# Kernel optimization log

Hardware: AMD Instinct MI355X
Metric: run time of the kernel (lower is better)

## Reference

```python
import jax, jax.numpy as jnp
import numpy as np

B, T, DM, DF, E, K = 4, 1024, 768, 3072, 8, 2


def setup_inputs() -> dict:
    key = jax.random.key(0)
    k0, k1, k2, k3 = jax.random.split(key, 4)
    x = jax.random.normal(k0, (B, T, DM), jnp.float32)
    Wg = jax.random.normal(k1, (DM, E), jnp.float32) * 0.02
    W1 = jax.random.normal(k2, (E, DM, DF), jnp.float32) * 0.02
    b1 = jnp.zeros((E, DF), jnp.float32)
    W2 = jax.random.normal(k3, (E, DF, DM), jnp.float32) * 0.02
    b2 = jnp.zeros((E, DM), jnp.float32)
    return {"x": x, "Wg": Wg, "W1": W1, "b1": b1, "W2": W2, "b2": b2}


def reference(x, Wg, W1, b1, W2, b2):
    # --- flatten (s)equence x (t)oken -> S tokens of width m ---
    m = x.shape[-1]
    xs = x.reshape(-1, m)              # [S, m]
    S = xs.shape[0]
    n_exp = W1.shape[0]

    # --- top-k softmax gate: combine_weights [k,S], dispatch order sorted by expert ---
    logits = xs @ Wg                   # [S, E]
    probs = jax.nn.softmax(logits, axis=-1)
    topv, topi = jax.lax.top_k(probs, K)                 # [S, K]
    cw = topv / jnp.sum(topv, axis=-1, keepdims=True)    # renormalize top-k
    combine_weights = cw.T                               # [K, S]

    # slot layout: slot = j*S + s (matches rerouted_output.reshape(k, S, m))
    eid_flat = topi.T.reshape(-1)                        # [S*K] expert id per slot
    dispatch_mask = jnp.argsort(eid_flat)                # stable sort by expert == chunked order
    e_sorted = eid_flat[dispatch_mask]                   # [S*K] sorted expert ids

    # --- dispatch: gather token rows (dispatch_mask % S indexes the token) ---
    dispatched = xs[dispatch_mask % S]                   # [S*K, m]

    # --- experts: per-expert FFN; loop over fixed small expert count, masked combine ---
    expert_outputs = jnp.zeros_like(dispatched)
    for e in range(n_exp):
        sel = (e_sorted == e)[:, None].astype(dispatched.dtype)
        h = jax.nn.relu(dispatched @ W1[e] + b1[e])      # [S*K, DF]
        expert_outputs = expert_outputs + sel * (h @ W2[e] + b2[e])

    # --- scatter back to slot order, then weighted combine over k ---
    rerouted = jnp.zeros((S * K, m), expert_outputs.dtype).at[dispatch_mask].set(expert_outputs)
    rerouted = rerouted.reshape(K, S, m)
    combined = jnp.einsum('ks,ksm->sm', combine_weights, rerouted)
    return combined.reshape(x.shape).astype(x.dtype)
```

## Files before the change

kernel.cpp:

```cpp
#include <hip/hip_runtime.h>
#include <math.h>

typedef short short8 __attribute__((ext_vector_type(8)));
typedef float f32x4 __attribute__((ext_vector_type(4)));
typedef unsigned short u16;
typedef unsigned int u32;

#define S_TOK 4096
#define DM 768
#define DF 3072
#define NE 8
#define NSLOT (S_TOK*2)
#define PSLOT 9216
#define MBMAX 72
#define MB64  144

#define WS_COUNTS   0
#define WS_CURSOR   512
#define WS_OFFS     1024
#define WS_MBE      1088
#define WS_EID      2048
#define WS_GW       (WS_EID + NSLOT*4)
#define WS_POS      (WS_GW  + NSLOT*4)
#define WS_TOK      (WS_POS + NSLOT*4)
#define CTRL_BYTES  262144

#define AS1 __attribute__((address_space(1)))
#define AS3 __attribute__((address_space(3)))
#define GLDS16(g, s) __builtin_amdgcn_global_load_lds((const AS1 u32*)(g), (AS3 u32*)(s), 16, 0, 0)

__device__ inline u16 f2b(float f){
    u32 u = __builtin_bit_cast(u32, f);
    u32 r = (u + 0x7fffu + ((u >> 16) & 1u)) >> 16;
    return (u16)r;
}
__device__ inline short8 ldcvt8f(const float* p){
    float4 a = *(const float4*)p;
    float4 b = *(const float4*)(p + 4);
    short8 v;
    v[0]=(short)f2b(a.x); v[1]=(short)f2b(a.y); v[2]=(short)f2b(a.z); v[3]=(short)f2b(a.w);
    v[4]=(short)f2b(b.x); v[5]=(short)f2b(b.y); v[6]=(short)f2b(b.z); v[7]=(short)f2b(b.w);
    return v;
}

#define GATE_BLOCKS 128
__global__ __launch_bounds__(256) void gate_kernel(const float* __restrict__ x, const float* __restrict__ Wg,
                                                   int* __restrict__ eid, float* __restrict__ gw,
                                                   int* __restrict__ counts){
    __shared__ int lh[NE];
    int t = threadIdx.x;
    if (t < NE) lh[t] = 0;
    __syncthreads();
    int wv = t >> 6, l = t & 63;
    int wgid = blockIdx.x*4 + wv;
    const int NW = GATE_BLOCKS*4;

    for (int s = wgid; s < S_TOK; s += NW){
        float acc[NE];
#pragma unroll
        for (int e = 0; e < NE; e++) acc[e] = 0.f;
        const float* xr = x + (size_t)s * DM;
#pragma unroll
        for (int i = 0; i < DM/64; i++){
            int d = l + 64*i;
            float xv = xr[d];
            float4 w0 = *(const float4*)(Wg + d*NE);
            float4 w1 = *(const float4*)(Wg + d*NE + 4);
            acc[0] += xv*w0.x; acc[1] += xv*w0.y; acc[2] += xv*w0.z; acc[3] += xv*w0.w;
            acc[4] += xv*w1.x; acc[5] += xv*w1.y; acc[6] += xv*w1.z; acc[7] += xv*w1.w;
        }
#pragma unroll
        for (int e = 0; e < NE; e++){
#pragma unroll
            for (int off = 32; off; off >>= 1) acc[e] += __shfl_down(acc[e], off);
        }
        if (l == 0){
            int i1 = 0; float v1 = acc[0];
            for (int e = 1; e < NE; e++) if (acc[e] > v1){ v1 = acc[e]; i1 = e; }
            int i2 = -1; float v2 = -1e30f;
            for (int e = 0; e < NE; e++) if (e != i1 && acc[e] > v2){ v2 = acc[e]; i2 = e; }
            float w0, w1;
            if (i2 < 0){ i2 = (i1 + 1) & 7; w0 = 1.f; w1 = 0.f; }
            else {
                float e2 = expf(v2 - v1);
                w0 = 1.f / (1.f + e2);
                w1 = e2 / (1.f + e2);
            }
            eid[2*s]   = i1; gw[2*s]   = w0;
            eid[2*s+1] = i2; gw[2*s+1] = w1;
            atomicAdd(&lh[i1], 1);
            atomicAdd(&lh[i2], 1);
        }
    }
    __syncthreads();
    if (t < NE && lh[t] > 0) atomicAdd(&counts[t*16], lh[t]);
}

__global__ void offsets_kernel(const int* __restrict__ counts, int* __restrict__ offs,
                               int* __restrict__ cursor, int* __restrict__ mbe){
    if (threadIdx.x == 0 && blockIdx.x == 0){
        int P = 0;
        for (int e = 0; e < NE; e++){
            offs[e] = P; cursor[e*16] = P;
            int padded = ((counts[e*16] + 127) >> 7) << 7;
            for (int mb = P >> 7; mb < (P + padded) >> 7; mb++) mbe[mb] = e;
            P += padded;
        }
        offs[NE] = P;
        for (int mb = P >> 7; mb < MBMAX; mb++) mbe[mb] = -1;
    }
}

__global__ __launch_bounds__(256) void scatter_kernel(const int* __restrict__ eid, int* __restrict__ cursor,
                                                      const int* __restrict__ counts, const int* __restrict__ offs,
                                                      const int* __restrict__ mbe,
                                                      int* __restrict__ tok_of, int* __restrict__ pos_of){
    __shared__ int lh[NE];
    __shared__ int base[NE];
    int t = threadIdx.x;
    if (t < NE) lh[t] = 0;
    __syncthreads();
    int i = blockIdx.x*256 + t;
    int e = 0, r = 0;
    if (i < NSLOT){
        e = eid[i];
        if (e < 0) e = 0; if (e > 7) e = 7;
        r = atomicAdd(&lh[e], 1);
    }
    __syncthreads();
    if (t < NE) base[t] = (lh[t] > 0) ? atomicAdd(&cursor[t*16], lh[t]) : 0;
    __syncthreads();
    if (i < NSLOT){
        int p = base[e] + r;
        if (p < 0) p = 0; if (p >= PSLOT) p = PSLOT - 1;
        tok_of[p] = i >> 1;
        pos_of[i] = p;
    }
    int p = i;
    int pe = mbe[p >> 7];
    if (pe < 0){ tok_of[p] = 0; }
    else if (p >= offs[pe] + counts[pe*16]){ tok_of[p] = 0; }
}

__global__ __launch_bounds__(256) void cvtx_kernel(const float* __restrict__ x, u16* __restrict__ xb,
                                                   int* __restrict__ counts, int* __restrict__ cursor){
    if (blockIdx.x == 0 && threadIdx.x < 128){ counts[threadIdx.x] = 0; cursor[threadIdx.x] = 0; }
    int i = (blockIdx.x*256 + threadIdx.x)*8;
    *(short8*)&xb[i] = ldcvt8f(&x[i]);
}

__global__ __launch_bounds__(256) void cvtshuf_kernel(const float* __restrict__ W, u16* __restrict__ Ws,
                                                      int Kd, int Nd){
    int kbn = Kd >> 5;
    int kb = blockIdx.x % kbn;
    int nb = blockIdx.x / kbn;
    int e  = blockIdx.y;
    const float* Wp = W + (size_t)e * Kd * Nd;
    u16* Wsp       = Ws + (size_t)e * Kd * Nd;
    int t = threadIdx.x;
    __shared__ u16 sh[32*136];
#pragma unroll
    for (int i = 0; i < 2; i++){
        int c = t + 256*i;
        int k = c >> 4, nc = c & 15;
        *(short8*)&sh[k*136 + nc*8] = ldcvt8f(&Wp[(size_t)(kb*32 + k)*Nd + nb*128 + nc*8]);
    }
    __syncthreads();
    int w = t >> 6, l = t & 63;
#pragma unroll
    for (int o = 0; o < 2; o++){
        int nt = 2*w + o;
        int n = nt*16 + (l & 15);
        short8 v;
#pragma unroll
        for (int j = 0; j < 8; j++) v[j] = (short)sh[((l >> 4)*8 + j)*136 + n];
        *(short8*)&Wsp[(size_t)(((nb*8 + nt) * kbn + kb) * 512) + l*8] = v;
    }
}

__global__ __launch_bounds__(256) void gemm1u_kernel(const u16* __restrict__ xb, const int* __restrict__ tok_of,
                                                     const int* __restrict__ mbe, const u16* __restrict__ W1s,
                                                     const float* __restrict__ b1, u16* __restrict__ h){
    const int KB = DM/32;
    const int KB2 = DM/64;
    int bid = blockIdx.x;
    int by = bid % 24, mb = bid / 24;
    int e = mbe[mb];
    if (e < 0) return;
    int m0 = mb*128, n0 = by*128;

    int t = threadIdx.x;
    int w = t >> 6, l = t & 63;
    int wm = w & 1, wn = w >> 1;

    __shared__ u16 As[128*72];
    __shared__ u16 Bs[2*2*8*512];

    int row0 = t >> 2, kc = t & 3;
    const u16* a0 = xb + (size_t)tok_of[m0 + row0]*DM + kc*8;
    const u16* a1 = xb + (size_t)tok_of[m0 + row0 + 64]*DM + kc*8;
    u16* as0 = &As[row0*72 + kc*8];
    u16* as1 = &As[(row0 + 64)*72 + kc*8];

    const u16* bbase = W1s + (size_t)e*DM*DF + (size_t)(((n0 >> 4) + 2*w)*KB)*512 + l*8;

    f32x4 acc[4][4];
#pragma unroll
    for (int i = 0; i < 4; i++)
#pragma unroll
        for (int j = 0; j < 4; j++) acc[i][j] = (f32x4){0.f,0.f,0.f,0.f};

    {
        short8 p0 = *(const short8*)a0;
        short8 p1 = *(const short8*)(a0 + 32);
        short8 p2 = *(const short8*)a1;
        short8 p3 = *(const short8*)(a1 + 32);
        *(short8*)as0 = p0; *(short8*)(as0 + 32) = p1;
        *(short8*)as1 = p2; *(short8*)(as1 + 32) = p3;
        GLDS16(bbase,                            &Bs[(2*w)*512]);
        GLDS16(bbase + 512,                      &Bs[4096 + (2*w)*512]);
        GLDS16(bbase + (size_t)KB*512,           &Bs[(2*w+1)*512]);
        GLDS16(bbase + (size_t)KB*512 + 512,     &Bs[4096 + (2*w+1)*512]);
    }
    __syncthreads();

    int c = 0;
    short8 av0a, av0b, av1a, av1b;
    for (int kb2 = 0; kb2 < KB2; kb2++){
        if (kb2 + 1 < KB2){
            GLDS16(bbase + (size_t)(2*kb2+2)*512,                     &Bs[(c^1)*8192 + (2*w)*512]);
            GLDS16(bbase + (size_t)(2*kb2+3)*512,                     &Bs[(c^1)*8192 + 4096 + (2*w)*512]);
            GLDS16(bbase + (size_t)KB*512 + (size_t)(2*kb2+2)*512,    &Bs[(c^1)*8192 + (2*w+1)*512]);
            GLDS16(bbase + (size_t)KB*512 + (size_t)(2*kb2+3)*512,    &Bs[(c^1)*8192 + 4096 + (2*w+1)*512]);
            av0a = *(const short8*)(a0 + (kb2+1)*64);
            av0b = *(const short8*)(a0 + (kb2+1)*64 + 32);
            av1a = *(const short8*)(a1 + (kb2+1)*64);
            av1b = *(const short8*)(a1 + (kb2+1)*64 + 32);
        }
#pragma unroll
        for (int ks = 0; ks < 2; ks++){
            short8 af[4], bf[4];
#pragma unroll
            for (int mt = 0; mt < 4; mt++)
                af[mt] = *(const short8*)&As[(wm*64 + mt*16 + (l & 15))*72 + ks*32 + (l >> 4)*8];
#pragma unroll
            for (int nt = 0; nt < 4; nt++)
                bf[nt] = *(const short8*)&Bs[c*8192 + ks*4096 + (wn*4 + nt)*512 + l*8];
#pragma unroll
            for (int mt = 0; mt < 4; mt++)
#pragma unroll
                for (int nt = 0; nt < 4; nt++)
                    acc[mt][nt] = __builtin_amdgcn_mfma_f32_16x16x32_bf16(af[mt], bf[nt], acc[mt][nt], 0, 0, 0);
        }
        __syncthreads();
        if (kb2 + 1 < KB2){
            *(short8*)as0 = av0a; *(short8*)(as0 + 32) = av0b;
            *(short8*)as1 = av1a; *(short8*)(as1 + 32) = av1b;
            __syncthreads();
        }
        c ^= 1;
    }

#pragma unroll
    for (int nt = 0; nt < 4; nt++){
        int col = n0 + wn*64 + nt*16 + (l & 15);
        float bv = b1[e*DF + col];
#pragma unroll
        for (int mt = 0; mt < 4; mt++){
#pragma unroll
            for (int r = 0; r < 4; r++){
                int grow = m0 + wm*64 + mt*16 + (l >> 4)*4 + r;
                float v = acc[mt][nt][r] + bv;
                v = v > 0.f ? v : 0.f;
                h[(size_t)grow*DF + col] = f2b(v);
            }
        }
    }
}

__global__ __launch_bounds__(256) void gemm2u_kernel(const u16* __restrict__ h, const int* __restrict__ mbe,
                                                     const u16* __restrict__ W2s, const float* __restrict__ b2,
                                                     float* __restrict__ y){
    const int KB = DF/32;
    const int KB2 = DF/64;
    int bid = blockIdx.x;
    int mb = bid % MB64;
    int by = bid / MB64;
    int e = mbe[mb >> 1];
    if (e < 0) return;
    int m0 = mb*64, n0 = by*128;

    int t = threadIdx.x;
    int w = t >> 6, l = t & 63;
    int wm = w & 1, wn = w >> 1;

    __shared__ u16 As[64*72];
    __shared__ u16 Bs[2*2*8*512];

    int row0 = t >> 2, kc = t & 3;
    const u16* a0 = h + (size_t)(m0 + row0)*DF + kc*8;
    u16* as0 = &As[row0*72 + kc*8];

    const u16* bbase = W2s + (size_t)e*DF*DM + (size_t)(((n0 >> 4) + 2*w)*KB)*512 + l*8;

    f32x4 acc[2][4];
#pragma unroll
    for (int i = 0; i < 2; i++)
#pragma unroll
        for (int j = 0; j < 4; j++) acc[i][j] = (f32x4){0.f,0.f,0.f,0.f};

    {
        short8 p0 = *(const short8*)a0;
        short8 p1 = *(const short8*)(a0 + 32);
        *(short8*)as0 = p0; *(short8*)(as0 + 32) = p1;
        GLDS16(bbase,                            &Bs[(2*w)*512]);
        GLDS16(bbase + 512,                      &Bs[4096 + (2*w)*512]);
        GLDS16(bbase + (size_t)KB*512,           &Bs[(2*w+1)*512]);
        GLDS16(bbase + (size_t)KB*512 + 512,     &Bs[4096 + (2*w+1)*512]);
    }
    __syncthreads();

    int c = 0;
    short8 av0a, av0b;
    for (int kb2 = 0; kb2 < KB2; kb2++){
        if (kb2 + 1 < KB2){
            GLDS16(bbase + (size_t)(2*kb2+2)*512,                     &Bs[(c^1)*8192 + (2*w)*512]);
            GLDS16(bbase + (size_t)(2*kb2+3)*512,                     &Bs[(c^1)*8192 + 4096 + (2*w)*512]);
            GLDS16(bbase + (size_t)KB*512 + (size_t)(2*kb2+2)*512,    &Bs[(c^1)*8192 + (2*w+1)*512]);
            GLDS16(bbase + (size_t)KB*512 + (size_t)(2*kb2+3)*512,    &Bs[(c^1)*8192 + 4096 + (2*w+1)*512]);
            av0a = *(const short8*)(a0 + (kb2+1)*64);
            av0b = *(const short8*)(a0 + (kb2+1)*64 + 32);
        }
#pragma unroll
        for (int ks = 0; ks < 2; ks++){
            short8 af[2], bf[4];
#pragma unroll
            for (int mt = 0; mt < 2; mt++)
                af[mt] = *(const short8*)&As[(wm*32 + mt*16 + (l & 15))*72 + ks*32 + (l >> 4)*8];
#pragma unroll
            for (int nt = 0; nt < 4; nt++)
                bf[nt] = *(const short8*)&Bs[c*8192 + ks*4096 + (wn*4 + nt)*512 + l*8];
#pragma unroll
            for (int mt = 0; mt < 2; mt++)
#pragma unroll
                for (int nt = 0; nt < 4; nt++)
                    acc[mt][nt] = __builtin_amdgcn_mfma_f32_16x16x32_bf16(af[mt], bf[nt], acc[mt][nt], 0, 0, 0);
        }
        __syncthreads();
        if (kb2 + 1 < KB2){
            *(short8*)as0 = av0a; *(short8*)(as0 + 32) = av0b;
            __syncthreads();
        }
        c ^= 1;
    }

#pragma unroll
    for (int nt = 0; nt < 4; nt++){
        int col = n0 + wn*64 + nt*16 + (l & 15);
        float bv = b2[e*DM + col];
#pragma unroll
        for (int mt = 0; mt < 2; mt++){
#pragma unroll
            for (int r = 0; r < 4; r++){
                int grow = m0 + wm*32 + mt*16 + (l >> 4)*4 + r;
                y[(size_t)grow*DM + col] = acc[mt][nt][r] + bv;
            }
        }
    }
}

__global__ __launch_bounds__(256) void combine_kernel(const float* __restrict__ y, const int* __restrict__ pos_of,
                                                      const float* __restrict__ gw, float* __restrict__ out){
    int i = blockIdx.x*256 + threadIdx.x;
    int s = i / (DM/4);
    int c4 = (i - s*(DM/4))*4;
    int p0 = pos_of[2*s], p1 = pos_of[2*s+1];
    float w0 = gw[2*s], w1 = gw[2*s+1];
    float4 a = *(const float4*)&y[(size_t)p0*DM + c4];
    float4 b = *(const float4*)&y[(size_t)p1*DM + c4];
    float4 o;
    o.x = w0*a.x + w1*b.x;
    o.y = w0*a.y + w1*b.y;
    o.z = w0*a.z + w1*b.z;
    o.w = w0*a.w + w1*b.w;
    *(float4*)&out[(size_t)s*DM + c4] = o;
}

__global__ __launch_bounds__(256) void fallback_kernel(const float* __restrict__ x, const float* __restrict__ Wg,
                                                       const float* __restrict__ W1, const float* __restrict__ b1,
                                                       const float* __restrict__ W2, const float* __restrict__ b2,
                                                       float* __restrict__ out){
    int s = blockIdx.x;
    int t = threadIdx.x;
    __shared__ float xr[DM];
    __shared__ float hl[DF];
    __shared__ float yl[DM];
    __shared__ float lacc[4*NE];
    __shared__ int   sel_e[2];
    __shared__ float sel_w[2];

    for (int i = t; i < DM; i += 256){ xr[i] = x[(size_t)s*DM + i]; yl[i] = 0.f; }
    __syncthreads();

    float acc[NE];
#pragma unroll
    for (int e = 0; e < NE; e++) acc[e] = 0.f;
    for (int d = t*3; d < t*3 + 3; d++){
        float xv = xr[d];
#pragma unroll
        for (int e = 0; e < NE; e++) acc[e] += xv * Wg[d*NE + e];
    }
#pragma unroll
    for (int e = 0; e < NE; e++){
#pragma unroll
        for (int off = 32; off; off >>= 1) acc[e] += __shfl_down(acc[e], off);
    }
    if ((t & 63) == 0){
        int wv = t >> 6;
#pragma unroll
        for (int e = 0; e < NE; e++) lacc[wv*NE + e] = acc[e];
    }
    __syncthreads();
    if (t == 0){
        float lg[NE];
#pragma unroll
        for (int e = 0; e < NE; e++) lg[e] = lacc[e] + lacc[NE + e] + lacc[2*NE + e] + lacc[3*NE + e];
        int i1 = 0; float v1 = lg[0];
        for (int e = 1; e < NE; e++) if (lg[e] > v1){ v1 = lg[e]; i1 = e; }
        int i2 = -1; float v2 = -1e30f;
        for (int e = 0; e < NE; e++) if (e != i1 && lg[e] > v2){ v2 = lg[e]; i2 = e; }
        if (i2 < 0){ i2 = (i1 + 1) & 7; sel_w[0] = 1.f; sel_w[1] = 0.f; }
        else {
            float e2 = expf(v2 - v1);
            sel_w[0] = 1.f / (1.f + e2);
            sel_w[1] = e2 / (1.f + e2);
        }
        sel_e[0] = i1; sel_e[1] = i2;
    }
    __syncthreads();

    for (int kk = 0; kk < 2; kk++){
        int e = sel_e[kk];
        float wgt = sel_w[kk];
        const float* w1p = W1 + (size_t)e * DM * DF;
        for (int j = t; j < DF; j += 256){
            float a = b1[e*DF + j];
            for (int k = 0; k < DM; k++) a += xr[k] * w1p[(size_t)k*DF + j];
            hl[j] = a > 0.f ? a : 0.f;
        }
        __syncthreads();
        const float* w2p = W2 + (size_t)e * DF * DM;
        for (int c = t; c < DM; c += 256){
            float a = b2[e*DM + c];
            for (int k = 0; k < DF; k++) a += hl[k] * w2p[(size_t)k*DM + c];
            yl[c] += wgt * a;
        }
        __syncthreads();
    }
    for (int c = t; c < DM; c += 256) out[(size_t)s*DM + c] = yl[c];
}

extern "C" void kernel_launch(void* const* d_in, const int* in_sizes, int n_in,
                              void* d_out, int out_size, void* d_ws, size_t ws_size,
                              hipStream_t stream) {
    const float* x  = (const float*)d_in[0];
    const float* Wg = (const float*)d_in[1];
    const float* W1 = (const float*)d_in[2];
    const float* b1 = (const float*)d_in[3];
    const float* W2 = (const float*)d_in[4];
    const float* b2 = (const float*)d_in[5];
    float* out = (float*)d_out;

    char* ws = (char*)d_ws;
    int*   counts = (int*)(ws + WS_COUNTS);
    int*   cursor = (int*)(ws + WS_CURSOR);
    int*   offs   = (int*)(ws + WS_OFFS);
    int*   mbe    = (int*)(ws + WS_MBE);
    int*   eid    = (int*)(ws + WS_EID);
    float* gw     = (float*)(ws + WS_GW);
    int*   pos_of = (int*)(ws + WS_POS);
    int*   tok_of = (int*)(ws + WS_TOK);

    const size_t xbB = (size_t)S_TOK*DM*2;
    const size_t wB  = (size_t)NE*DM*DF*2;
    const size_t hB  = (size_t)PSLOT*DF*2;
    const size_t need = CTRL_BYTES + xbB + 2*wB + hB;

    if (ws_size < need){
        fallback_kernel<<<S_TOK, 256, 0, stream>>>(x, Wg, W1, b1, W2, b2, out);
        return;
    }

    u16* xb  = (u16*)(ws + CTRL_BYTES);
    u16* W1s = (u16*)(ws + CTRL_BYTES + xbB);
    u16* W2s = (u16*)(ws + CTRL_BYTES + xbB + wB);
    u16* h   = (u16*)(ws + CTRL_BYTES + xbB + 2*wB);
    float* yb = (float*)(ws + CTRL_BYTES + xbB);

    cvtx_kernel<<<S_TOK*DM/8/256, 256, 0, stream>>>(x, xb, counts, cursor);
    cvtshuf_kernel<<<dim3((DM/32)*(DF/128), NE), 256, 0, stream>>>(W1, W1s, DM, DF);
    cvtshuf_kernel<<<dim3((DF/32)*(DM/128), NE), 256, 0, stream>>>(W2, W2s, DF, DM);
    gate_kernel<<<GATE_BLOCKS, 256, 0, stream>>>(x, Wg, eid, gw, counts);
    offsets_kernel<<<1, 1, 0, stream>>>(counts, offs, cursor, mbe);
    scatter_kernel<<<PSLOT/256, 256, 0, stream>>>(eid, cursor, counts, offs, mbe, tok_of, pos_of);

    gemm1u_kernel<<<MBMAX*24, 256, 0, stream>>>(xb, tok_of, mbe, W1s, b1, h);
    gemm2u_kernel<<<6*MB64, 256, 0, stream>>>(h, mbe, W2s, b2, yb);
    combine_kernel<<<(S_TOK*(DM/4))/256, 256, 0, stream>>>(yb, pos_of, gw, out);
}
```

Before: 382.5 us.

## Use 128-row tiles and triple-buffered B pipeline in second expert GEMM

The second expert GEMM now uses 128x128 output tiles per block instead of 64x128, and streams B through a three-stage LDS ring with async global-to-LDS loads issued two stages ahead. Explicit vmcnt/lgkmcnt waits with raw s_barrier replace __syncthreads. The aim is more reuse of each B tile and more latency hiding. In exchange, the grid halves to 432 blocks, which may underfill the GPU, and accumulator registers double.

```diff
diff --git a/kernel.cpp b/kernel.cpp
--- a/kernel.cpp
+++ b/kernel.cpp
@@ -13,7 +13,6 @@
 #define NSLOT (S_TOK*2)
 #define PSLOT 9216
 #define MBMAX 72
-#define MB64  144
 
 #define WS_COUNTS   0
 #define WS_CURSOR   512
@@ -278,91 +277,113 @@
     }
 }
 
-__global__ __launch_bounds__(256) void gemm2u_kernel(const u16* __restrict__ h, const int* __restrict__ mbe,
+__global__ __launch_bounds__(256) void gemm2p_kernel(const u16* __restrict__ h, const int* __restrict__ mbe,
                                                      const u16* __restrict__ W2s, const float* __restrict__ b2,
                                                      float* __restrict__ y){
     const int KB = DF/32;
-    const int KB2 = DF/64;
+    const int NT = DF/64;
     int bid = blockIdx.x;
-    int mb = bid % MB64;
-    int by = bid / MB64;
-    int e = mbe[mb >> 1];
+    int mb = bid % MBMAX;
+    int by = bid / MBMAX;
+    int e = mbe[mb];
     if (e < 0) return;
-    int m0 = mb*64, n0 = by*128;
+    int m0 = mb*128, n0 = by*128;
 
     int t = threadIdx.x;
     int w = t >> 6, l = t & 63;
     int wm = w & 1, wn = w >> 1;
 
-    __shared__ u16 As[64*72];
-    __shared__ u16 Bs[2*2*8*512];
+    __shared__ u16 As[128*72];
+    __shared__ u16 Bs[3*2*8*512];
 
     int row0 = t >> 2, kc = t & 3;
     const u16* a0 = h + (size_t)(m0 + row0)*DF + kc*8;
+    const u16* a1 = h + (size_t)(m0 + row0 + 64)*DF + kc*8;
     u16* as0 = &As[row0*72 + kc*8];
+    u16* as1 = &As[(row0 + 64)*72 + kc*8];
 
     const u16* bbase = W2s + (size_t)e*DF*DM + (size_t)(((n0 >> 4) + 2*w)*KB)*512 + l*8;
 
-    f32x4 acc[2][4];
-#pragma unroll
-    for (int i = 0; i < 2; i++)
+#define STB2(kb2, buf) do{ \
+    GLDS16(bbase + (size_t)(2*(kb2))*512,                   &Bs[(buf)*8192 + (2*w)*512]); \
+    GLDS16(bbase + (size_t)(2*(kb2)+1)*512,                 &Bs[(buf)*8192 + 4096 + (2*w)*512]); \
+    GLDS16(bbase + (size_t)KB*512 + (size_t)(2*(kb2))*512,  &Bs[(buf)*8192 + (2*w+1)*512]); \
+    GLDS16(bbase + (size_t)KB*512 + (size_t)(2*(kb2)+1)*512,&Bs[(buf)*8192 + 4096 + (2*w+1)*512]); \
+}while(0)
+
+    f32x4 acc[4][4];
+#pragma unroll
+    for (int i = 0; i < 4; i++)
 #pragma unroll
         for (int j = 0; j < 4; j++) acc[i][j] = (f32x4){0.f,0.f,0.f,0.f};
 
-    {
-        short8 p0 = *(const short8*)a0;
-        short8 p1 = *(const short8*)(a0 + 32);
-        *(short8*)as0 = p0; *(short8*)(as0 + 32) = p1;
-        GLDS16(bbase,                            &Bs[(2*w)*512]);
-        GLDS16(bbase + 512,                      &Bs[4096 + (2*w)*512]);
-        GLDS16(bbase + (size_t)KB*512,           &Bs[(2*w+1)*512]);
-        GLDS16(bbase + (size_t)KB*512 + 512,     &Bs[4096 + (2*w+1)*512]);
-    }
-    __syncthreads();
-
-    int c = 0;
-    short8 av0a, av0b;
-    for (int kb2 = 0; kb2 < KB2; kb2++){
-        if (kb2 + 1 < KB2){
-            GLDS16(bbase + (size_t)(2*kb2+2)*512,                     &Bs[(c^1)*8192 + (2*w)*512]);
-            GLDS16(bbase + (size_t)(2*kb2+3)*512,                     &Bs[(c^1)*8192 + 4096 + (2*w)*512]);
-            GLDS16(bbase + (size_t)KB*512 + (size_t)(2*kb2+2)*512,    &Bs[(c^1)*8192 + (2*w+1)*512]);
-            GLDS16(bbase + (size_t)KB*512 + (size_t)(2*kb2+3)*512,    &Bs[(c^1)*8192 + 4096 + (2*w+1)*512]);
-            av0a = *(const short8*)(a0 + (kb2+1)*64);
-            av0b = *(const short8*)(a0 + (kb2+1)*64 + 32);
-        }
+    short8 av0a = *(const short8*)a0;
+    short8 av0b = *(const short8*)(a0 + 32);
+    short8 av1a = *(const short8*)a1;
+    short8 av1b = *(const short8*)(a1 + 32);
+    STB2(0, 0);
+    STB2(1, 1);
+    *(short8*)as0 = av0a; *(short8*)(as0 + 32) = av0b;
+    *(short8*)as1 = av1a; *(short8*)(as1 + 32) = av1b;
+    av0a = *(const short8*)(a0 + 64);
+    av0b = *(const short8*)(a0 + 96);
+    av1a = *(const short8*)(a1 + 64);
+    av1b = *(const short8*)(a1 + 96);
+    __builtin_amdgcn_sched_barrier(0);
+    asm volatile("s_waitcnt vmcnt(8) lgkmcnt(0)" ::: "memory");
+    __builtin_amdgcn_sched_barrier(0);
+    __builtin_amdgcn_s_barrier();
+
+    int cb = 0, sb = 2;
+    for (int kt = 0; kt < NT; kt++){
+        if (kt + 2 < NT) STB2(kt + 2, sb);
 #pragma unroll
         for (int ks = 0; ks < 2; ks++){
-            short8 af[2], bf[4];
-#pragma unroll
-            for (int mt = 0; mt < 2; mt++)
-                af[mt] = *(const short8*)&As[(wm*32 + mt*16 + (l & 15))*72 + ks*32 + (l >> 4)*8];
+            short8 af[4], bf[4];
+#pragma unroll
+            for (int mt = 0; mt < 4; mt++)
+                af[mt] = *(const short8*)&As[(wm*64 + mt*16 + (l & 15))*72 + ks*32 + (l >> 4)*8];
 #pragma unroll
             for (int nt = 0; nt < 4; nt++)
-                bf[nt] = *(const short8*)&Bs[c*8192 + ks*4096 + (wn*4 + nt)*512 + l*8];
-#pragma unroll
-            for (int mt = 0; mt < 2; mt++)
+                bf[nt] = *(const short8*)&Bs[cb*8192 + ks*4096 + (wn*4 + nt)*512 + l*8];
+#pragma unroll
+            for (int mt = 0; mt < 4; mt++)
 #pragma unroll
                 for (int nt = 0; nt < 4; nt++)
                     acc[mt][nt] = __builtin_amdgcn_mfma_f32_16x16x32_bf16(af[mt], bf[nt], acc[mt][nt], 0, 0, 0);
         }
-        __syncthreads();
-        if (kb2 + 1 < KB2){
+        __builtin_amdgcn_sched_barrier(0);
+        asm volatile("s_waitcnt vmcnt(4) lgkmcnt(0)" ::: "memory");
+        __builtin_amdgcn_sched_barrier(0);
+        __builtin_amdgcn_s_barrier();
+        if (kt + 1 < NT){
             *(short8*)as0 = av0a; *(short8*)(as0 + 32) = av0b;
-            __syncthreads();
-        }
-        c ^= 1;
-    }
+            *(short8*)as1 = av1a; *(short8*)(as1 + 32) = av1b;
+            if (kt + 2 < NT){
+                av0a = *(const short8*)(a0 + (kt+2)*64);
+                av0b = *(const short8*)(a0 + (kt+2)*64 + 32);
+                av1a = *(const short8*)(a1 + (kt+2)*64);
+                av1b = *(const short8*)(a1 + (kt+2)*64 + 32);
+            }
+            __builtin_amdgcn_sched_barrier(0);
+            asm volatile("s_waitcnt lgkmcnt(0)" ::: "memory");
+            __builtin_amdgcn_sched_barrier(0);
+            __builtin_amdgcn_s_barrier();
+        }
+        cb = (cb == 2) ? 0 : cb + 1;
+        sb = (sb == 2) ? 0 : sb + 1;
+    }
+#undef STB2
 
 #pragma unroll
     for (int nt = 0; nt < 4; nt++){
         int col = n0 + wn*64 + nt*16 + (l & 15);
         float bv = b2[e*DM + col];
 #pragma unroll
-        for (int mt = 0; mt < 2; mt++){
+        for (int mt = 0; mt < 4; mt++){
 #pragma unroll
             for (int r = 0; r < 4; r++){
-                int grow = m0 + wm*32 + mt*16 + (l >> 4)*4 + r;
+                int grow = m0 + wm*64 + mt*16 + (l >> 4)*4 + r;
                 y[(size_t)grow*DM + col] = acc[mt][nt][r] + bv;
             }
         }
@@ -505,6 +526,6 @@
     scatter_kernel<<<PSLOT/256, 256, 0, stream>>>(eid, cursor, counts, offs, mbe, tok_of, pos_of);
 
     gemm1u_kernel<<<MBMAX*24, 256, 0, stream>>>(xb, tok_of, mbe, W1s, b1, h);
-    gemm2u_kernel<<<6*MB64, 256, 0, stream>>>(h, mbe, W2s, b2, yb);
+    gemm2p_kernel<<<6*MBMAX, 256, 0, stream>>>(h, mbe, W2s, b2, yb);
     combine_kernel<<<(S_TOK*(DM/4))/256, 256, 0, stream>>>(yb, pos_of, gw, out);
 }
```

After: 345.7 us. -9.6%, faster.
